# Kernel optimization log

Hardware: AMD Instinct MI355X
Metric: run time of the kernel (lower is better)

Reference implementation:

```python
import jax, jax.numpy as jnp
import numpy as np

B, S, H, NH, EHH, L = 8, 4, 50, 200, 400, 2
HID = 128
FDIM = 44 + 20 + 15          # 79: atom one-hot + amino-acid one-hot + position one-hot
EDIM = 2 * FDIM + 3          # h_i, h_j, distance, bond, t -> 161


def setup_inputs() -> dict:
    key = jax.random.key(0)
    ks = jax.random.split(key, 32)
    inp = {}
    inp["t"] = jax.random.uniform(ks[0], (B,), dtype=jnp.float32)
    inp["x_h"] = jax.random.normal(ks[1], (B, S, H, 3), dtype=jnp.float32)
    inp["x_heavy"] = jax.random.normal(ks[2], (B, 1, NH, 3), dtype=jnp.float32)
    inp["bond_matrix_h_heavy"] = (jax.random.uniform(ks[3], (B, H, NH)) < 0.02).astype(jnp.float32)
    inp["edge_mask_h_heavy"] = jnp.ones((B, H, NH), jnp.float32)
    inp["edge_mask_h_h"] = jnp.ones((B, EHH), jnp.float32)
    inp["atom_mask"] = jnp.ones((B, H, 1), jnp.float32)
    sc = 0.02
    shapes = {"W1": (L, EDIM, HID), "b1": (L, HID), "W2": (L, HID, HID), "b2": (L, HID),
              "Wc1": (L, HID, HID), "bc1": (L, HID), "Wc2": (L, HID, 1),
              "Wn1": (L, FDIM + HID, HID), "bn1": (L, HID), "Wn2": (L, HID, FDIM), "bn2": (L, FDIM)}
    for i, (n, s) in enumerate(shapes.items()):
        inp[n] = jax.random.normal(ks[4 + i], s, dtype=jnp.float32) * sc
    inp["peptide_seq"] = jax.random.randint(ks[20], (B, 15), 0, 20)
    inp["atom_labels_heavy"] = jax.random.randint(ks[21], (B, NH), 0, 44)
    inp["atom_labels_h"] = jax.random.randint(ks[22], (B, H), 0, 44)
    inp["amino_acid_pos_heavy"] = jax.random.randint(ks[23], (B, NH), 1, 16)
    inp["amino_acid_pos_h"] = jax.random.randint(ks[24], (B, H), 1, 16)
    inp["edges_h_h"] = jax.random.randint(ks[25], (B, EHH, 2), 0, H)
    inp["bound_atom"] = jax.random.randint(ks[26], (B, H), 0, NH)
    return inp


def _embed(labels, pos, peptide_seq):
    # one_hot(atom,44) ++ one_hot(seq[pos-1],20) ++ one_hot(pos-1,15)
    aa = jnp.take_along_axis(peptide_seq, pos - 1, axis=1)
    return jnp.concatenate([jax.nn.one_hot(labels, 44, dtype=jnp.float32),
                            jax.nn.one_hot(aa, 20, dtype=jnp.float32),
                            jax.nn.one_hot(pos - 1, 15, dtype=jnp.float32)], axis=-1)


def _gather_nodes(feat, idx):
    # feat [B,S,N,D], idx [B,E] -> [B,S,E,D]
    return jnp.take_along_axis(feat, idx[:, None, :, None], axis=2)


def _seg(data, ids, n):
    # data [B,S,E,D], ids [B,E] -> scatter-add over edges -> [B,S,n,D]
    f = jax.vmap(lambda d, i: jax.ops.segment_sum(jnp.swapaxes(d, 0, 1), i, num_segments=n))
    return jnp.swapaxes(f(data, ids), 1, 2)


def _forward(t, x_h, x_heavy, bond_hm, em_hheavy, em_hh, atom_mask,
             W1, b1, W2, b2, Wc1, bc1, Wc2, Wn1, bn1, Wn2, bn2,
             peptide_seq, atom_labels_heavy, atom_labels_h, pos_heavy, pos_h,
             edges_h_h, bound_atom):
    Bq, Sq, Hq, _ = x_h.shape
    Nh = x_heavy.shape[2]
    xhv = jnp.broadcast_to(x_heavy, (Bq, Sq, Nh, 3))
    emb_h = _embed(atom_labels_h, pos_h, peptide_seq)          # [B,H,79]
    emb_hv = _embed(atom_labels_heavy, pos_heavy, peptide_seq)  # [B,NH,79]
    # absolute coords: x_h relative to its bound heavy atom
    x_h_abs = x_h + jnp.take_along_axis(xhv, bound_atom[:, None, :, None], axis=2)
    x = jnp.concatenate([x_h_abs, xhv], axis=2)                 # [B,S,N,3]
    feat = jnp.concatenate([emb_h, emb_hv], axis=1)             # [B,N,79]
    feat = jnp.broadcast_to(feat[:, None], (Bq, Sq) + feat.shape[1:])
    bond = jnp.concatenate([jnp.zeros((Bq, Hq, Hq), bond_hm.dtype), bond_hm], axis=-1)  # [B,H,N]
    # edge indices: sparse h-h edges, then full h x heavy grid (row-major, cols offset by H)
    grid_r = jnp.repeat(jnp.arange(Hq), Nh)
    grid_c = Hq + jnp.tile(jnp.arange(Nh), Hq)
    edge_row = jnp.concatenate([edges_h_h[..., 0], jnp.broadcast_to(grid_r, (Bq, Hq * Nh))], axis=-1)
    edge_col = jnp.concatenate([edges_h_h[..., 1], jnp.broadcast_to(grid_c, (Bq, Hq * Nh))], axis=-1)
    emask = jnp.concatenate([em_hh, em_hheavy.reshape(Bq, -1)], axis=-1)[:, None, :, None]  # [B,1,E,1]
    bond_e = jax.vmap(lambda bm, r, c: bm[r, c])(bond, edge_row, edge_col)[:, None, :, None]
    x0 = x
    for l in range(W1.shape[0]):
        xi = _gather_nodes(x, edge_row)
        xj = _gather_nodes(x, edge_col)
        diff = xi - xj                                          # [B,S,E,3]
        dist = jnp.linalg.norm(diff, axis=-1, keepdims=True)    # [B,S,E,1]
        hi = _gather_nodes(feat, edge_row)
        hj = _gather_nodes(feat, edge_col)
        t_e = jnp.broadcast_to(t[:, None, None, None], dist.shape)
        ef = jnp.concatenate([hi, hj, dist, jnp.broadcast_to(bond_e, dist.shape), t_e], axis=-1)
        m = jax.nn.silu(ef @ W1[l] + b1[l])
        m = jax.nn.silu(m @ W2[l] + b2[l]) * emask              # masked messages [B,S,E,HID]
        cw = jax.nn.silu(m @ Wc1[l] + bc1[l]) @ Wc2[l]          # [B,S,E,1]
        agg_x = _seg(diff * cw, edge_row, Hq)                   # [B,S,H,3]
        agg_m = _seg(m, edge_row, Hq)                           # [B,S,H,HID]
        h_h = feat[:, :, :Hq]
        h_out = h_h + jax.nn.silu(jnp.concatenate([h_h, agg_m], axis=-1) @ Wn1[l] + bn1[l]) @ Wn2[l] + bn2[l]
        x = jnp.concatenate([x[:, :, :Hq] + agg_x, x[:, :, Hq:]], axis=2)
        feat = jnp.concatenate([h_out, feat[:, :, Hq:]], axis=2)
    pred = (x[:, :, :Hq] - x0[:, :, :Hq]) * atom_mask[:, None, :, :]
    return pred


def reference(t, x_h, x_heavy, bond_matrix_h_heavy, edge_mask_h_heavy, edge_mask_h_h, atom_mask,
              W1, b1, W2, b2, Wc1, bc1, Wc2, Wn1, bn1, Wn2, bn2,
              peptide_seq, atom_labels_heavy, atom_labels_h, amino_acid_pos_heavy, amino_acid_pos_h,
              edges_h_h, bound_atom):
    return _forward(t, x_h, x_heavy, bond_matrix_h_heavy, edge_mask_h_heavy, edge_mask_h_h, atom_mask,
                    W1, b1, W2, b2, Wc1, bc1, Wc2, Wn1, bn1, Wn2, bn2,
                    peptide_seq, atom_labels_heavy, atom_labels_h, amino_acid_pos_heavy, amino_acid_pos_h,
                    edges_h_h, bound_atom)
```

## Files before the change

### kernel.cpp

```cpp
#include <hip/hip_runtime.h>
#include <math.h>

#define B_     8
#define S_     4
#define H_     50
#define NH_    200
#define EHH_   400
#define L_     2
#define HID_   128
#define FDIM_  79
#define EDIM_  161
#define NN_    250
#define NROW_  1600
#define BS_    32
#define FS_    80
#define MSTR_  136
#define NDIM_  207
#define HVB_   1600

#define OFF_FEATH  0
#define OFF_X      128000
#define OFF_X0H    160000
#define OFF_HHCOL  166400
#define OFF_HHEM   169600
#define OFF_HHOFF  172800
#define OFF_AGG0   173312
#define AGGSTRIDE_ 211200
#define OFF_AGG1   384512
#define OFF_HIW1   595712
#define OFF_HJW1   800512
#define OFF_WP     1414912

typedef __attribute__((ext_vector_type(8))) short short8;
typedef __attribute__((ext_vector_type(4))) float f32x4;

__device__ __forceinline__ float silu_(float v) {
    return v * __builtin_amdgcn_rcpf(1.0f + __expf(-v));
}
__device__ __forceinline__ unsigned short f2bf(float f) {
    unsigned int u = __float_as_uint(f);
    unsigned int r = (u + 0x7fffu + ((u >> 16) & 1u)) >> 16;
    return (unsigned short)r;
}

#define HV_BLKS_    1600
#define PACK_BLKS_  256
#define SORT_BLKS_  8
#define HROW_BLKS_  200
#define FEAT_BLKS_  125
#define XI_BLKS_    32
#define SETUP_BLKS_ (HV_BLKS_ + PACK_BLKS_ + SORT_BLKS_ + HROW_BLKS_ + FEAT_BLKS_ + XI_BLKS_)

__global__ __launch_bounds__(256) void k_setup(
    const float* __restrict__ x_h, const float* __restrict__ x_hv,
    const int* __restrict__ bound,
    const int* __restrict__ ehh, const float* __restrict__ em_hh,
    const float* __restrict__ W1, const float* __restrict__ b1,
    const float* __restrict__ t_in,
    const float* __restrict__ W2, const float* __restrict__ Wc1,
    const int* __restrict__ lab_h, const int* __restrict__ pos_h,
    const int* __restrict__ lab_hv, const int* __restrict__ pos_hv,
    const int* __restrict__ pep,
    float* __restrict__ feat_h,
    float* __restrict__ x, float* __restrict__ x0h,
    int* __restrict__ hhcol, float* __restrict__ hhem, int* __restrict__ hhoff,
    float* __restrict__ hiW1, float* __restrict__ hjW1,
    unsigned short* __restrict__ Wp)
{
    int blk = blockIdx.x, t = threadIdx.x;
    if (blk < HV_BLKS_) {
        int g = blk*256 + t;
        int l = g / 204800;
        int r = g - l*204800;
        int node = r >> 7, col = r & 127;
        int b = node / NH_;
        int label = lab_hv[node], pos = pos_hv[node];
        int aa = pep[b*15 + pos - 1];
        const float* W1l = W1 + l*EDIM_*HID_;
        float hj = W1l[(FDIM_ + label)*HID_ + col]
                 + W1l[(FDIM_ + 44 + aa)*HID_ + col]
                 + W1l[(FDIM_ + 64 + pos - 1)*HID_ + col];
        hjW1[(size_t)(HVB_ + l*1600 + node)*HID_ + col] = hj;
        return;
    }
    blk -= HV_BLKS_;
    if (blk < PACK_BLKS_) {
        int g = blk*256 + t;
        int idx = g & 16383;
        int lm  = g >> 14;
        int l = lm >> 1, mat = lm & 1;
        int j   = idx & 7;
        int l15 = (idx >> 3) & 15;
        int qq  = (idx >> 7) & 3;
        int nt  = (idx >> 9) & 7;
        int kc  = (idx >> 12) & 3;
        int n = nt*16 + l15;
        int k = kc*32 + qq*8 + j;
        const float* W = (mat == 0 ? W2 : Wc1) + l*HID_*HID_;
        Wp[g] = f2bf(W[k*HID_ + n]);
        return;
    }
    blk -= PACK_BLKS_;
    if (blk < SORT_BLKS_) {
        int b = blk;
        __shared__ int scnt[64];
        __shared__ int srow[EHH_], scol[EHH_];
        __shared__ float sem[EHH_];
        if (t < 64) scnt[t] = 0;
        __syncthreads();
        for (int e = t; e < EHH_; e += 256) {
            int r = ehh[(b*EHH_ + e)*2 + 0];
            srow[e] = r;
            scol[e] = ehh[(b*EHH_ + e)*2 + 1];
            sem[e]  = em_hh[b*EHH_ + e];
            atomicAdd(&scnt[r], 1);
        }
        __syncthreads();
        if (t == 0) {
            int acc = 0;
            for (int i = 0; i < H_; ++i) { int v = scnt[i]; scnt[i] = acc; acc += v; }
        }
        __syncthreads();
        if (t < 51) hhoff[b*64 + t] = (t < H_) ? scnt[t] : EHH_;
        __syncthreads();
        for (int e = t; e < EHH_; e += 256) {
            int r = srow[e];
            int pos = atomicAdd(&scnt[r], 1);
            hhcol[b*EHH_ + pos] = scol[e];
            hhem [b*EHH_ + pos] = sem[e];
        }
        return;
    }
    blk -= SORT_BLKS_;
    if (blk < HROW_BLKS_) {
        int g = blk*256 + t;
        int node = g >> 7, col = g & 127;
        int b = node / H_;
        int label = lab_h[node], pos = pos_h[node];
        int aa = pep[b*15 + pos - 1];
        const float* W1l = W1;
        float hi = W1l[label*HID_ + col]
                 + W1l[(44 + aa)*HID_ + col]
                 + W1l[(64 + pos - 1)*HID_ + col]
                 + b1[col]
                 + t_in[b] * W1l[160*HID_ + col];
        float hj = W1l[(FDIM_ + label)*HID_ + col]
                 + W1l[(FDIM_ + 44 + aa)*HID_ + col]
                 + W1l[(FDIM_ + 64 + pos - 1)*HID_ + col];
        int h = node % H_;
        #pragma unroll
        for (int s = 0; s < S_; ++s) {
            int row = (b*S_ + s)*H_ + h;
            hiW1[(size_t)row*HID_ + col] = hi;
            hjW1[(size_t)row*HID_ + col] = hj;
        }
        return;
    }
    blk -= HROW_BLKS_;
    if (blk < FEAT_BLKS_) {
        int g = blk*256 + t;
        int node = g / FS_, f = g % FS_;
        int b = node / H_, h = node % H_;
        int label = lab_h[node], pos = pos_h[node];
        int aa = pep[b*15 + pos - 1];
        float v = 0.f;
        if (f < 44)      v = (f == label)          ? 1.0f : 0.0f;
        else if (f < 64) v = ((f - 44) == aa)      ? 1.0f : 0.0f;
        else if (f < 79) v = ((f - 64) == pos - 1) ? 1.0f : 0.0f;
        #pragma unroll
        for (int s = 0; s < S_; ++s)
            feat_h[((b*S_ + s)*H_ + h)*FS_ + f] = v;
        return;
    }
    blk -= FEAT_BLKS_;
    {
        int g = blk*256 + t;
        if (g >= BS_*NN_) return;
        int bs = g / NN_, n = g % NN_;
        int b = bs / S_;
        if (n < H_) {
            int ba = bound[b*H_ + n];
            for (int d = 0; d < 3; ++d) {
                float v = x_h[(bs*H_ + n)*3 + d] + x_hv[(b*NH_ + ba)*3 + d];
                x[g*4 + d] = v;
                x0h[(bs*H_ + n)*4 + d] = v;
            }
        } else {
            int nh = n - H_;
            for (int d = 0; d < 3; ++d) x[g*4 + d] = x_hv[(b*NH_ + nh)*3 + d];
        }
    }
}

__global__ __launch_bounds__(512) void k_edge_mlp(
    const float* __restrict__ x, const float* __restrict__ hiW1,
    const float* __restrict__ hjW1,
    const int* __restrict__ hhcol, const float* __restrict__ hhem,
    const int* __restrict__ hhoff,
    const float* __restrict__ em_hv, const float* __restrict__ bond_in,
    const float* __restrict__ W1,
    const float* __restrict__ b2, const float* __restrict__ bc1,
    const float* __restrict__ Wc2,
    const unsigned short* __restrict__ Wp, int l,
    float* __restrict__ aggx, float* __restrict__ aggm)
{
    __shared__ unsigned short s_wp[2*16384];
    __shared__ unsigned short s_m[8][16][MSTR_];
    __shared__ float s_hi[2][HID_];
    __shared__ float s_cc[5][HID_];
    __shared__ float s_mr[2][4][HID_];
    __shared__ float s_xr[2][4][4];

    const int t = threadIdx.x, lane = t & 63, w = t >> 6;
    const int l15 = lane & 15, q = lane >> 4;
    const int r  = w >> 2;
    const int wr = w & 3;
    const int node0 = blockIdx.x*2;
    const int node  = node0 + r;
    const int bs = node / H_, h = node - bs*H_;
    const int b  = bs / S_;

    {
        const float4* src = (const float4*)(Wp + (size_t)l*32768);
        float4* dst = (float4*)s_wp;
        #pragma unroll
        for (int i = 0; i < 8; ++i) dst[t + i*512] = src[t + i*512];
    }
    const float* W1l = W1 + l*EDIM_*HID_;
    if (t < 128) {
        s_hi[0][t] = hiW1[(size_t)node0*HID_ + t];
    } else if (t < 256) {
        int c = t - 128;
        s_hi[1][c] = hiW1[(size_t)(node0 + 1)*HID_ + c];
    } else if (t < 384) {
        int c = t - 256;
        s_cc[0][c] = W1l[158*HID_ + c];
        s_cc[3][c] = bc1[l*HID_ + c];
    } else {
        int c = t - 384;
        s_cc[1][c] = W1l[159*HID_ + c];
        s_cc[2][c] = b2 [l*HID_ + c];
        s_cc[4][c] = Wc2[l*HID_ + c];
    }

    const int hh0 = hhoff[b*64 + h];
    const int cnt = hhoff[b*64 + h + 1] - hh0;
    const int E   = cnt + NH_;
    const int NT  = (E + 15) >> 4;

    const float xi0 = x[(bs*NN_ + h)*4 + 0];
    const float xi1 = x[(bs*NN_ + h)*4 + 1];
    const float xi2 = x[(bs*NN_ + h)*4 + 2];

    auto gather = [&](int e, float& d0, float& d1, float& d2,
                      float& dist, float& bnd, float& em, int& jj) {
        if (e < E) {
            int col;
            if (e < cnt) {
                col = hhcol[b*EHH_ + hh0 + e];
                em  = hhem [b*EHH_ + hh0 + e];
                jj  = bs*H_ + col;
            } else {
                int cc = e - cnt;
                col = H_ + cc;
                em  = em_hv [(b*H_ + h)*NH_ + cc];
                bnd = bond_in[(b*H_ + h)*NH_ + cc];
                jj  = HVB_ + l*1600 + b*NH_ + cc;
            }
            d0 = xi0 - x[(bs*NN_ + col)*4 + 0];
            d1 = xi1 - x[(bs*NN_ + col)*4 + 1];
            d2 = xi2 - x[(bs*NN_ + col)*4 + 2];
            dist = sqrtf(d0*d0 + d1*d1 + d2*d2);
        }
    };

    float macc[8] = {0.f,0.f,0.f,0.f,0.f,0.f,0.f,0.f};
    float xacc = 0.f;
    __syncthreads();

    float cd0=0.f, cd1=0.f, cd2=0.f, cdist=0.f, cbnd=0.f, cem=0.f;
    int   cjj = bs*H_;
    if (lane < 16) gather(wr*16 + lane, cd0, cd1, cd2, cdist, cbnd, cem, cjj);
    float distb = __shfl(cdist, l15, 64);
    float bndb  = __shfl(cbnd,  l15, 64);
    int   jjb   = __shfl(cjj,   l15, 64);
    float4 pr[8];
    {
        const float* pj = hjW1 + (size_t)jjb*HID_ + q*8;
        #pragma unroll
        for (int kc = 0; kc < 4; ++kc) {
            pr[2*kc]   = *(const float4*)(pj + kc*32);
            pr[2*kc+1] = *(const float4*)(pj + kc*32 + 4);
        }
    }

    for (int ti = wr; ti < NT; ti += 4) {
        const int nx = ti + 4;
        const bool hasNext = (nx < NT);

        float nd0=0.f, nd1=0.f, nd2=0.f, ndist=0.f, nbnd=0.f, nem=0.f;
        int   njj = bs*H_;
        if (hasNext && lane < 16)
            gather(nx*16 + lane, nd0, nd1, nd2, ndist, nbnd, nem, njj);

        short8 afrag[4];
        #pragma unroll
        for (int kc = 0; kc < 4; ++kc) {
            int k0 = kc*32 + q*8;
            float4 c0 = pr[2*kc];
            float4 c1 = pr[2*kc+1];
            float4 h0 = *(const float4*)&s_hi[r][k0];
            float4 h1 = *(const float4*)&s_hi[r][k0 + 4];
            float4 wa0= *(const float4*)&s_cc[0][k0];
            float4 wa1= *(const float4*)&s_cc[0][k0 + 4];
            float4 wb0= *(const float4*)&s_cc[1][k0];
            float4 wb1= *(const float4*)&s_cc[1][k0 + 4];
            short8 fr;
            fr[0] = (short)f2bf(silu_(h0.x + c0.x + distb*wa0.x + bndb*wb0.x));
            fr[1] = (short)f2bf(silu_(h0.y + c0.y + distb*wa0.y + bndb*wb0.y));
            fr[2] = (short)f2bf(silu_(h0.z + c0.z + distb*wa0.z + bndb*wb0.z));
            fr[3] = (short)f2bf(silu_(h0.w + c0.w + distb*wa0.w + bndb*wb0.w));
            fr[4] = (short)f2bf(silu_(h1.x + c1.x + distb*wa1.x + bndb*wb1.x));
            fr[5] = (short)f2bf(silu_(h1.y + c1.y + distb*wa1.y + bndb*wb1.y));
            fr[6] = (short)f2bf(silu_(h1.z + c1.z + distb*wa1.z + bndb*wb1.z));
            fr[7] = (short)f2bf(silu_(h1.w + c1.w + distb*wa1.w + bndb*wb1.w));
            afrag[kc] = fr;
        }

        float ndistb = 0.f, nbndb = 0.f;
        if (hasNext) {
            ndistb = __shfl(ndist, l15, 64);
            nbndb  = __shfl(nbnd,  l15, 64);
            int njjb = __shfl(njj, l15, 64);
            const float* pj = hjW1 + (size_t)njjb*HID_ + q*8;
            #pragma unroll
            for (int kc = 0; kc < 4; ++kc) {
                pr[2*kc]   = *(const float4*)(pj + kc*32);
                pr[2*kc+1] = *(const float4*)(pj + kc*32 + 4);
            }
        }

        float em4[4];
        #pragma unroll
        for (int rr = 0; rr < 4; ++rr) em4[rr] = __shfl(cem, q*4 + rr, 64);
        #pragma unroll
        for (int nt = 0; nt < 8; ++nt) {
            float bias = s_cc[2][nt*16 + l15];
            f32x4 c = {bias, bias, bias, bias};
            #pragma unroll
            for (int kc = 0; kc < 4; ++kc) {
                short8 bf = *(const short8*)&s_wp[((kc*8 + nt)*64 + lane)*8];
                c = __builtin_amdgcn_mfma_f32_16x16x32_bf16(afrag[kc], bf, c, 0, 0, 0);
            }
            #pragma unroll
            for (int rr = 0; rr < 4; ++rr) {
                float mv = silu_(c[rr]) * em4[rr];
                s_m[w][q*4 + rr][nt*16 + l15] = f2bf(mv);
                macc[nt] += mv;
            }
        }
        __builtin_amdgcn_wave_barrier();

        short8 af2[4];
        #pragma unroll
        for (int kc = 0; kc < 4; ++kc)
            af2[kc] = *(const short8*)&s_m[w][l15][kc*32 + q*8];
        float p[4] = {0.f, 0.f, 0.f, 0.f};
        #pragma unroll
        for (int nt = 0; nt < 8; ++nt) {
            float bias = s_cc[3][nt*16 + l15];
            f32x4 c = {bias, bias, bias, bias};
            #pragma unroll
            for (int kc = 0; kc < 4; ++kc) {
                short8 bf = *(const short8*)&s_wp[16384 + ((kc*8 + nt)*64 + lane)*8];
                c = __builtin_amdgcn_mfma_f32_16x16x32_bf16(af2[kc], bf, c, 0, 0, 0);
            }
            float wcv = s_cc[4][nt*16 + l15];
            #pragma unroll
            for (int rr = 0; rr < 4; ++rr)
                p[rr] += silu_(c[rr]) * wcv;
        }
        #pragma unroll
        for (int m = 1; m < 16; m <<= 1) {
            #pragma unroll
            for (int rr = 0; rr < 4; ++rr) p[rr] += __shfl_xor(p[rr], m, 64);
        }
        #pragma unroll
        for (int rr = 0; rr < 4; ++rr) {
            float sd0 = __shfl(cd0, q*4 + rr, 64);
            float sd1 = __shfl(cd1, q*4 + rr, 64);
            float sd2 = __shfl(cd2, q*4 + rr, 64);
            if (l15 < 3) {
                float dsel = (l15 == 0) ? sd0 : ((l15 == 1) ? sd1 : sd2);
                xacc += dsel * p[rr];
            }
        }
        __builtin_amdgcn_wave_barrier();

        cd0 = nd0; cd1 = nd1; cd2 = nd2; cem = nem;
        distb = ndistb; bndb = nbndb;
    }

    #pragma unroll
    for (int nt = 0; nt < 8; ++nt) {
        macc[nt] += __shfl_xor(macc[nt], 16, 64);
        macc[nt] += __shfl_xor(macc[nt], 32, 64);
    }
    if (q == 0) {
        #pragma unroll
        for (int nt = 0; nt < 8; ++nt) s_mr[r][wr][nt*16 + l15] = macc[nt];
    }
    xacc += __shfl_xor(xacc, 16, 64);
    xacc += __shfl_xor(xacc, 32, 64);
    if (q == 0 && l15 < 3) s_xr[r][wr][l15] = xacc;
    __syncthreads();
    if (t < 256) {
        int rr = t >> 7, col = t & 127;
        aggm[(size_t)(node0 + rr)*HID_ + col] =
            s_mr[rr][0][col] + s_mr[rr][1][col] + s_mr[rr][2][col] + s_mr[rr][3][col];
    } else if (t < 262) {
        int ix = t - 256, rr = ix / 3, d = ix - rr*3;
        aggx[(node0 + rr)*4 + d] =
            s_xr[rr][0][d] + s_xr[rr][1][d] + s_xr[rr][2][d] + s_xr[rr][3][d];
    }
}

__global__ __launch_bounds__(128) void k_update(
    float* __restrict__ feat_h, float* __restrict__ x,
    const float* __restrict__ aggm, const float* __restrict__ aggx,
    const float* __restrict__ Wn1, const float* __restrict__ bn1,
    const float* __restrict__ Wn2, const float* __restrict__ bn2, int l,
    const float* __restrict__ W1, const float* __restrict__ b1,
    const float* __restrict__ t_in,
    float* __restrict__ hiW1, float* __restrict__ hjW1, int do_w1,
    const float* __restrict__ x0h, const float* __restrict__ amask,
    float* __restrict__ out)
{
    __shared__ float s_in[8][NDIM_ + 1];
    __shared__ float s_u[8][HID_ + 1];
    int node0 = blockIdx.x * 8;
    int t = threadIdx.x;
    for (int idx = t; idx < 8*(NDIM_ + 1); idx += 128) {
        int g = idx / (NDIM_ + 1), k = idx % (NDIM_ + 1);
        float v = 0.f;
        if (k < FDIM_)      v = feat_h[(node0 + g)*FS_ + k];
        else if (k < NDIM_) v = aggm[(size_t)(node0 + g)*HID_ + (k - FDIM_)];
        s_in[g][k] = v;
    }
    __syncthreads();
    const float* Wn1l = Wn1 + l*NDIM_*HID_;
    float acc[8];
    float bv = bn1[l*HID_ + t];
    #pragma unroll
    for (int g = 0; g < 8; ++g) acc[g] = bv;
    for (int k = 0; k < NDIM_; ++k) {
        float wv = Wn1l[k*HID_ + t];
        #pragma unroll
        for (int g = 0; g < 8; ++g) acc[g] += s_in[g][k] * wv;
    }
    #pragma unroll
    for (int g = 0; g < 8; ++g) s_u[g][t] = silu_(acc[g]);
    __syncthreads();
    if (t < FDIM_) {
        const float* Wn2l = Wn2 + l*HID_*FDIM_;
        float acc2[8];
        float b2v = bn2[l*FDIM_ + t];
        #pragma unroll
        for (int g = 0; g < 8; ++g) acc2[g] = b2v;
        for (int k = 0; k < HID_; ++k) {
            float wv = Wn2l[k*FDIM_ + t];
            #pragma unroll
            for (int g = 0; g < 8; ++g) acc2[g] += s_u[g][k] * wv;
        }
        #pragma unroll
        for (int g = 0; g < 8; ++g) {
            float nf = s_in[g][t] + acc2[g];
            feat_h[(node0 + g)*FS_ + t] = nf;
            s_in[g][t] = nf;
        }
    } else if (t >= 96 && t < 120) {
        int idx = t - 96, g = idx / 3, d = idx % 3;
        int node = node0 + g;
        int bs = node / H_, h = node % H_;
        float xv = x[(bs*NN_ + h)*4 + d] + aggx[node*4 + d];
        x[(bs*NN_ + h)*4 + d] = xv;
        if (!do_w1) {
            int b = bs / S_;
            out[node*3 + d] = (xv - x0h[node*4 + d]) * amask[b*H_ + h];
        }
    }
    if (!do_w1) return;
    __syncthreads();
    {
        const float* W1n = W1 + (l + 1)*EDIM_*HID_;
        float w160 = W1n[160*HID_ + t];
        float b1v  = b1[(l + 1)*HID_ + t];
        float hia[8], hja[8];
        #pragma unroll
        for (int g = 0; g < 8; ++g) { hia[g] = 0.f; hja[g] = 0.f; }
        for (int f = 0; f < FDIM_; ++f) {
            float wi = W1n[f*HID_ + t];
            float wj = W1n[(FDIM_ + f)*HID_ + t];
            #pragma unroll
            for (int g = 0; g < 8; ++g) {
                float v = s_in[g][f];
                hia[g] += v * wi;
                hja[g] += v * wj;
            }
        }
        #pragma unroll
        for (int g = 0; g < 8; ++g) {
            int node = node0 + g;
            int b = (node / H_) / S_;
            hiW1[(size_t)node*HID_ + t] = hia[g] + b1v + t_in[b]*w160;
            hjW1[(size_t)node*HID_ + t] = hja[g];
        }
    }
}

extern "C" void kernel_launch(void* const* d_in, const int* in_sizes, int n_in,
                              void* d_out, int out_size, void* d_ws, size_t ws_size,
                              hipStream_t stream)
{
    const float* t_in  = (const float*)d_in[0];
    const float* x_h   = (const float*)d_in[1];
    const float* x_hv  = (const float*)d_in[2];
    const float* bond  = (const float*)d_in[3];
    const float* em_hv = (const float*)d_in[4];
    const float* em_hh = (const float*)d_in[5];
    const float* amask = (const float*)d_in[6];
    const float* W1    = (const float*)d_in[7];
    const float* b1    = (const float*)d_in[8];
    const float* W2    = (const float*)d_in[9];
    const float* b2    = (const float*)d_in[10];
    const float* Wc1   = (const float*)d_in[11];
    const float* bc1   = (const float*)d_in[12];
    const float* Wc2   = (const float*)d_in[13];
    const float* Wn1   = (const float*)d_in[14];
    const float* bn1   = (const float*)d_in[15];
    const float* Wn2   = (const float*)d_in[16];
    const float* bn2   = (const float*)d_in[17];
    const int* pep     = (const int*)d_in[18];
    const int* lab_hv  = (const int*)d_in[19];
    const int* lab_h   = (const int*)d_in[20];
    const int* pos_hv  = (const int*)d_in[21];
    const int* pos_h   = (const int*)d_in[22];
    const int* ehh     = (const int*)d_in[23];
    const int* bound   = (const int*)d_in[24];

    float* ws     = (float*)d_ws;
    float* feat_h = ws + OFF_FEATH;
    float* x      = ws + OFF_X;
    float* x0h    = ws + OFF_X0H;
    int*   hhcol  = (int*)(ws + OFF_HHCOL);
    float* hhem   = ws + OFF_HHEM;
    int*   hhoff  = (int*)(ws + OFF_HHOFF);
    float* hiW1   = ws + OFF_HIW1;
    float* hjW1   = ws + OFF_HJW1;
    unsigned short* Wp = (unsigned short*)(ws + OFF_WP);

    hipLaunchKernelGGL(k_setup, dim3(SETUP_BLKS_), dim3(256), 0, stream,
                       x_h, x_hv, bound, ehh, em_hh,
                       W1, b1, t_in, W2, Wc1,
                       lab_h, pos_h, lab_hv, pos_hv, pep,
                       feat_h, x, x0h, hhcol, hhem, hhoff,
                       hiW1, hjW1, Wp);

    for (int l = 0; l < L_; ++l) {
        float* aggx_l = ws + OFF_AGG0 + (size_t)l*AGGSTRIDE_;
        float* aggm_l = aggx_l + 6400;
        hipLaunchKernelGGL(k_edge_mlp, dim3(NROW_/2), dim3(512), 0, stream,
                           x, hiW1, hjW1, hhcol, hhem, hhoff, em_hv, bond,
                           W1, b2, bc1, Wc2, Wp, l, aggx_l, aggm_l);
        int do_w1 = (l == 0);
        hipLaunchKernelGGL(k_update, dim3(200), dim3(128), 0, stream,
                           feat_h, x, aggm_l, aggx_l, Wn1, bn1, Wn2, bn2, l,
                           W1, b1, t_in, hiW1, hjW1, do_w1,
                           x0h, amask, (float*)d_out);
    }
}
```

Baseline: 384.9 us.

## Split k_update into more blocks with a two-way K-split reduction

The node-update kernel now handles 4 nodes per block instead of 8, using 256 threads and 400 blocks instead of 200 blocks of 128. The two halves of each block split the reduction dimension of every matmul (Wn1, Wn2 and the next-layer W1 projection) and combine partial sums through shared memory. The aim is more parallelism and occupancy on a small, latency-bound kernel. The cost is extra syncthreads and shared-memory reductions, and each weight row is now read by twice as many blocks.

```diff
diff --git a/kernel.cpp b/kernel.cpp
--- a/kernel.cpp
+++ b/kernel.cpp
@@ -425,7 +425,7 @@
     }
 }
 
-__global__ __launch_bounds__(128) void k_update(
+__global__ __launch_bounds__(256) void k_update(
     float* __restrict__ feat_h, float* __restrict__ x,
     const float* __restrict__ aggm, const float* __restrict__ aggx,
     const float* __restrict__ Wn1, const float* __restrict__ bn1,
@@ -436,11 +436,16 @@
     const float* __restrict__ x0h, const float* __restrict__ amask,
     float* __restrict__ out)
 {
-    __shared__ float s_in[8][NDIM_ + 1];
-    __shared__ float s_u[8][HID_ + 1];
-    int node0 = blockIdx.x * 8;
-    int t = threadIdx.x;
-    for (int idx = t; idx < 8*(NDIM_ + 1); idx += 128) {
+    __shared__ float s_in[4][NDIM_ + 1];
+    __shared__ float s_u [4][HID_ + 1];
+    __shared__ float s_p1[2][4][HID_];
+    __shared__ float s_p2[2][4][HID_];
+    const int node0 = blockIdx.x * 4;
+    const int t = threadIdx.x;
+    const int c  = t & 127;
+    const int kh = t >> 7;
+
+    for (int idx = t; idx < 4*(NDIM_ + 1); idx += 256) {
         int g = idx / (NDIM_ + 1), k = idx % (NDIM_ + 1);
         float v = 0.f;
         if (k < FDIM_)      v = feat_h[(node0 + g)*FS_ + k];
@@ -448,40 +453,53 @@
         s_in[g][k] = v;
     }
     __syncthreads();
-    const float* Wn1l = Wn1 + l*NDIM_*HID_;
-    float acc[8];
-    float bv = bn1[l*HID_ + t];
-    #pragma unroll
-    for (int g = 0; g < 8; ++g) acc[g] = bv;
-    for (int k = 0; k < NDIM_; ++k) {
-        float wv = Wn1l[k*HID_ + t];
-        #pragma unroll
-        for (int g = 0; g < 8; ++g) acc[g] += s_in[g][k] * wv;
-    }
-    #pragma unroll
-    for (int g = 0; g < 8; ++g) s_u[g][t] = silu_(acc[g]);
+
+    {
+        const float* Wn1l = Wn1 + l*NDIM_*HID_;
+        float acc[4] = {0.f, 0.f, 0.f, 0.f};
+        const int k0 = kh*104, k1 = kh ? NDIM_ : 104;
+        for (int k = k0; k < k1; ++k) {
+            float wv = Wn1l[k*HID_ + c];
+            #pragma unroll
+            for (int g = 0; g < 4; ++g) acc[g] += s_in[g][k] * wv;
+        }
+        #pragma unroll
+        for (int g = 0; g < 4; ++g) s_p1[kh][g][c] = acc[g];
+    }
     __syncthreads();
-    if (t < FDIM_) {
+    if (kh == 0) {
+        float bv = bn1[l*HID_ + c];
+        #pragma unroll
+        for (int g = 0; g < 4; ++g)
+            s_u[g][c] = silu_(s_p1[0][g][c] + s_p1[1][g][c] + bv);
+    }
+    __syncthreads();
+
+    if (c < FDIM_) {
         const float* Wn2l = Wn2 + l*HID_*FDIM_;
-        float acc2[8];
-        float b2v = bn2[l*FDIM_ + t];
-        #pragma unroll
-        for (int g = 0; g < 8; ++g) acc2[g] = b2v;
-        for (int k = 0; k < HID_; ++k) {
-            float wv = Wn2l[k*FDIM_ + t];
-            #pragma unroll
-            for (int g = 0; g < 8; ++g) acc2[g] += s_u[g][k] * wv;
-        }
-        #pragma unroll
-        for (int g = 0; g < 8; ++g) {
-            float nf = s_in[g][t] + acc2[g];
-            feat_h[(node0 + g)*FS_ + t] = nf;
-            s_in[g][t] = nf;
-        }
-    } else if (t >= 96 && t < 120) {
-        int idx = t - 96, g = idx / 3, d = idx % 3;
+        float a2[4] = {0.f, 0.f, 0.f, 0.f};
+        const int kk0 = kh*64, kk1 = kk0 + 64;
+        for (int k = kk0; k < kk1; ++k) {
+            float wv = Wn2l[k*FDIM_ + c];
+            #pragma unroll
+            for (int g = 0; g < 4; ++g) a2[g] += s_u[g][k] * wv;
+        }
+        #pragma unroll
+        for (int g = 0; g < 4; ++g) s_p1[kh][g][c] = a2[g];
+    }
+    __syncthreads();
+    if (kh == 0 && c < FDIM_) {
+        float b2v = bn2[l*FDIM_ + c];
+        #pragma unroll
+        for (int g = 0; g < 4; ++g) {
+            float nf = s_in[g][c] + s_p1[0][g][c] + s_p1[1][g][c] + b2v;
+            feat_h[(node0 + g)*FS_ + c] = nf;
+            s_in[g][c] = nf;
+        }
+    } else if (kh == 1 && c < 12) {
+        int g = c / 3, d = c - g*3;
         int node = node0 + g;
-        int bs = node / H_, h = node % H_;
+        int bs = node / H_, h = node - bs*H_;
         float xv = x[(bs*NN_ + h)*4 + d] + aggx[node*4 + d];
         x[(bs*NN_ + h)*4 + d] = xv;
         if (!do_w1) {
@@ -491,29 +509,38 @@
     }
     if (!do_w1) return;
     __syncthreads();
+
     {
         const float* W1n = W1 + (l + 1)*EDIM_*HID_;
-        float w160 = W1n[160*HID_ + t];
-        float b1v  = b1[(l + 1)*HID_ + t];
-        float hia[8], hja[8];
-        #pragma unroll
-        for (int g = 0; g < 8; ++g) { hia[g] = 0.f; hja[g] = 0.f; }
-        for (int f = 0; f < FDIM_; ++f) {
-            float wi = W1n[f*HID_ + t];
-            float wj = W1n[(FDIM_ + f)*HID_ + t];
-            #pragma unroll
-            for (int g = 0; g < 8; ++g) {
+        float hia[4] = {0.f,0.f,0.f,0.f}, hja[4] = {0.f,0.f,0.f,0.f};
+        const int f0 = kh*40, f1 = kh ? FDIM_ : 40;
+        for (int f = f0; f < f1; ++f) {
+            float wi = W1n[f*HID_ + c];
+            float wj = W1n[(FDIM_ + f)*HID_ + c];
+            #pragma unroll
+            for (int g = 0; g < 4; ++g) {
                 float v = s_in[g][f];
                 hia[g] += v * wi;
                 hja[g] += v * wj;
             }
         }
         #pragma unroll
-        for (int g = 0; g < 8; ++g) {
-            int node = node0 + g;
-            int b = (node / H_) / S_;
-            hiW1[(size_t)node*HID_ + t] = hia[g] + b1v + t_in[b]*w160;
-            hjW1[(size_t)node*HID_ + t] = hja[g];
+        for (int g = 0; g < 4; ++g) {
+            s_p1[kh][g][c] = hia[g];
+            s_p2[kh][g][c] = hja[g];
+        }
+        __syncthreads();
+        if (kh == 0) {
+            float w160 = W1n[160*HID_ + c];
+            float b1v  = b1[(l + 1)*HID_ + c];
+            #pragma unroll
+            for (int g = 0; g < 4; ++g) {
+                int node = node0 + g;
+                int b = (node / H_) / S_;
+                hiW1[(size_t)node*HID_ + c] =
+                    s_p1[0][g][c] + s_p1[1][g][c] + b1v + t_in[b]*w160;
+                hjW1[(size_t)node*HID_ + c] = s_p2[0][g][c] + s_p2[1][g][c];
+            }
         }
     }
 }
@@ -573,7 +600,7 @@
                            x, hiW1, hjW1, hhcol, hhem, hhoff, em_hv, bond,
                            W1, b2, bc1, Wc2, Wp, l, aggx_l, aggm_l);
         int do_w1 = (l == 0);
-        hipLaunchKernelGGL(k_update, dim3(200), dim3(128), 0, stream,
+        hipLaunchKernelGGL(k_update, dim3(400), dim3(256), 0, stream,
                            feat_h, x, aggm_l, aggx_l, Wn1, bn1, Wn2, bn2, l,
                            W1, b1, t_in, hiW1, hjW1, do_w1,
                            x0h, amask, (float*)d_out);
```

Measured after the change: 383.7 us. No clear change (-0.3%).

## Fuse node update into edge MLP kernel with double-buffered coordinates

Applied to the files above, without the earlier changes.

Merges the per-node update (Wn1/Wn2 MLP, coordinate update, next-layer W1 projections) into the tail of the edge kernel, so each layer is one launch. Aggregated messages feed the node MLP directly from shared memory instead of a global round-trip. Coordinates and the hi/hj projection buffers are double-buffered per layer to avoid read-after-write races across blocks. The cost is small per-block node work on 512 threads with extra syncs, and the update is spread over 800 blocks of 2 nodes instead of 200 blocks of 8, so weight reads are repeated more often.

```diff
diff --git a/kernel.cpp b/kernel.cpp
--- a/kernel.cpp
+++ b/kernel.cpp
@@ -19,17 +19,15 @@
 #define HVB_   1600
 
 #define OFF_FEATH  0
-#define OFF_X      128000
-#define OFF_X0H    160000
-#define OFF_HHCOL  166400
-#define OFF_HHEM   169600
-#define OFF_HHOFF  172800
-#define OFF_AGG0   173312
-#define AGGSTRIDE_ 211200
-#define OFF_AGG1   384512
-#define OFF_HIW1   595712
-#define OFF_HJW1   800512
-#define OFF_WP     1414912
+#define OFF_X0     128000
+#define OFF_X1     160000
+#define OFF_X0H    192000
+#define OFF_HHCOL  198400
+#define OFF_HHEM   201600
+#define OFF_HHOFF  204800
+#define OFF_HIW1   205312
+#define OFF_HJW1   614912
+#define OFF_WP     1434112
 
 typedef __attribute__((ext_vector_type(8))) short short8;
 typedef __attribute__((ext_vector_type(4))) float f32x4;
@@ -62,7 +60,7 @@
     const int* __restrict__ lab_hv, const int* __restrict__ pos_hv,
     const int* __restrict__ pep,
     float* __restrict__ feat_h,
-    float* __restrict__ x, float* __restrict__ x0h,
+    float* __restrict__ x0, float* __restrict__ x1, float* __restrict__ x0h,
     int* __restrict__ hhcol, float* __restrict__ hhem, int* __restrict__ hhoff,
     float* __restrict__ hiW1, float* __restrict__ hjW1,
     unsigned short* __restrict__ Wp)
@@ -182,18 +180,22 @@
             int ba = bound[b*H_ + n];
             for (int d = 0; d < 3; ++d) {
                 float v = x_h[(bs*H_ + n)*3 + d] + x_hv[(b*NH_ + ba)*3 + d];
-                x[g*4 + d] = v;
+                x0[g*4 + d] = v;
                 x0h[(bs*H_ + n)*4 + d] = v;
             }
         } else {
             int nh = n - H_;
-            for (int d = 0; d < 3; ++d) x[g*4 + d] = x_hv[(b*NH_ + nh)*3 + d];
+            for (int d = 0; d < 3; ++d) {
+                float v = x_hv[(b*NH_ + nh)*3 + d];
+                x0[g*4 + d] = v;
+                x1[g*4 + d] = v;
+            }
         }
     }
 }
 
 __global__ __launch_bounds__(512) void k_edge_mlp(
-    const float* __restrict__ x, const float* __restrict__ hiW1,
+    const float* __restrict__ xin, const float* __restrict__ hiW1g,
     const float* __restrict__ hjW1,
     const int* __restrict__ hhcol, const float* __restrict__ hhem,
     const int* __restrict__ hhoff,
@@ -202,7 +204,13 @@
     const float* __restrict__ b2, const float* __restrict__ bc1,
     const float* __restrict__ Wc2,
     const unsigned short* __restrict__ Wp, int l,
-    float* __restrict__ aggx, float* __restrict__ aggm)
+    const float* __restrict__ Wn1, const float* __restrict__ bn1,
+    const float* __restrict__ Wn2, const float* __restrict__ bn2,
+    const float* __restrict__ b1, const float* __restrict__ t_in,
+    float* __restrict__ feat_h, float* __restrict__ xout,
+    float* __restrict__ hiW1w, float* __restrict__ hjW1w,
+    const float* __restrict__ x0h, const float* __restrict__ amask,
+    float* __restrict__ out, int do_w1)
 {
     __shared__ unsigned short s_wp[2*16384];
     __shared__ unsigned short s_m[8][16][MSTR_];
@@ -219,6 +227,7 @@
     const int node  = node0 + r;
     const int bs = node / H_, h = node - bs*H_;
     const int b  = bs / S_;
+    const int hb = (l ? 4800 : 0) + bs*H_;
 
     {
         const float4* src = (const float4*)(Wp + (size_t)l*32768);
@@ -228,10 +237,10 @@
     }
     const float* W1l = W1 + l*EDIM_*HID_;
     if (t < 128) {
-        s_hi[0][t] = hiW1[(size_t)node0*HID_ + t];
+        s_hi[0][t] = hiW1g[(size_t)(l*1600 + node0)*HID_ + t];
     } else if (t < 256) {
         int c = t - 128;
-        s_hi[1][c] = hiW1[(size_t)(node0 + 1)*HID_ + c];
+        s_hi[1][c] = hiW1g[(size_t)(l*1600 + node0 + 1)*HID_ + c];
     } else if (t < 384) {
         int c = t - 256;
         s_cc[0][c] = W1l[158*HID_ + c];
@@ -248,9 +257,9 @@
     const int E   = cnt + NH_;
     const int NT  = (E + 15) >> 4;
 
-    const float xi0 = x[(bs*NN_ + h)*4 + 0];
-    const float xi1 = x[(bs*NN_ + h)*4 + 1];
-    const float xi2 = x[(bs*NN_ + h)*4 + 2];
+    const float xi0 = xin[(bs*NN_ + h)*4 + 0];
+    const float xi1 = xin[(bs*NN_ + h)*4 + 1];
+    const float xi2 = xin[(bs*NN_ + h)*4 + 2];
 
     auto gather = [&](int e, float& d0, float& d1, float& d2,
                       float& dist, float& bnd, float& em, int& jj) {
@@ -259,7 +268,7 @@
             if (e < cnt) {
                 col = hhcol[b*EHH_ + hh0 + e];
                 em  = hhem [b*EHH_ + hh0 + e];
-                jj  = bs*H_ + col;
+                jj  = hb + col;
             } else {
                 int cc = e - cnt;
                 col = H_ + cc;
@@ -267,9 +276,9 @@
                 bnd = bond_in[(b*H_ + h)*NH_ + cc];
                 jj  = HVB_ + l*1600 + b*NH_ + cc;
             }
-            d0 = xi0 - x[(bs*NN_ + col)*4 + 0];
-            d1 = xi1 - x[(bs*NN_ + col)*4 + 1];
-            d2 = xi2 - x[(bs*NN_ + col)*4 + 2];
+            d0 = xi0 - xin[(bs*NN_ + col)*4 + 0];
+            d1 = xi1 - xin[(bs*NN_ + col)*4 + 1];
+            d2 = xi2 - xin[(bs*NN_ + col)*4 + 2];
             dist = sqrtf(d0*d0 + d1*d1 + d2*d2);
         }
     };
@@ -279,7 +288,7 @@
     __syncthreads();
 
     float cd0=0.f, cd1=0.f, cd2=0.f, cdist=0.f, cbnd=0.f, cem=0.f;
-    int   cjj = bs*H_;
+    int   cjj = hb;
     if (lane < 16) gather(wr*16 + lane, cd0, cd1, cd2, cdist, cbnd, cem, cjj);
     float distb = __shfl(cdist, l15, 64);
     float bndb  = __shfl(cbnd,  l15, 64);
@@ -299,7 +308,7 @@
         const bool hasNext = (nx < NT);
 
         float nd0=0.f, nd1=0.f, nd2=0.f, ndist=0.f, nbnd=0.f, nem=0.f;
-        int   njj = bs*H_;
+        int   njj = hb;
         if (hasNext && lane < 16)
             gather(nx*16 + lane, nd0, nd1, nd2, ndist, nbnd, nem, njj);
 
@@ -414,106 +423,79 @@
     xacc += __shfl_xor(xacc, 32, 64);
     if (q == 0 && l15 < 3) s_xr[r][wr][l15] = xacc;
     __syncthreads();
-    if (t < 256) {
-        int rr = t >> 7, col = t & 127;
-        aggm[(size_t)(node0 + rr)*HID_ + col] =
-            s_mr[rr][0][col] + s_mr[rr][1][col] + s_mr[rr][2][col] + s_mr[rr][3][col];
-    } else if (t < 262) {
-        int ix = t - 256, rr = ix / 3, d = ix - rr*3;
-        aggx[(node0 + rr)*4 + d] =
-            s_xr[rr][0][d] + s_xr[rr][1][d] + s_xr[rr][2][d] + s_xr[rr][3][d];
-    }
-}
-
-__global__ __launch_bounds__(128) void k_update(
-    float* __restrict__ feat_h, float* __restrict__ x,
-    const float* __restrict__ aggm, const float* __restrict__ aggx,
-    const float* __restrict__ Wn1, const float* __restrict__ bn1,
-    const float* __restrict__ Wn2, const float* __restrict__ bn2, int l,
-    const float* __restrict__ W1, const float* __restrict__ b1,
-    const float* __restrict__ t_in,
-    float* __restrict__ hiW1, float* __restrict__ hjW1, int do_w1,
-    const float* __restrict__ x0h, const float* __restrict__ amask,
-    float* __restrict__ out)
-{
-    __shared__ float s_in[8][NDIM_ + 1];
-    __shared__ float s_u[8][HID_ + 1];
-    int node0 = blockIdx.x * 8;
-    int t = threadIdx.x;
-    for (int idx = t; idx < 8*(NDIM_ + 1); idx += 128) {
-        int g = idx / (NDIM_ + 1), k = idx % (NDIM_ + 1);
+
+    float* su = (float*)s_wp;
+    if (t < 416) {
+        int g = t / 208, k = t - g*208;
         float v = 0.f;
         if (k < FDIM_)      v = feat_h[(node0 + g)*FS_ + k];
-        else if (k < NDIM_) v = aggm[(size_t)(node0 + g)*HID_ + (k - FDIM_)];
-        s_in[g][k] = v;
-    }
-    __syncthreads();
-    const float* Wn1l = Wn1 + l*NDIM_*HID_;
-    float acc[8];
-    float bv = bn1[l*HID_ + t];
-    #pragma unroll
-    for (int g = 0; g < 8; ++g) acc[g] = bv;
-    for (int k = 0; k < NDIM_; ++k) {
-        float wv = Wn1l[k*HID_ + t];
-        #pragma unroll
-        for (int g = 0; g < 8; ++g) acc[g] += s_in[g][k] * wv;
-    }
-    #pragma unroll
-    for (int g = 0; g < 8; ++g) s_u[g][t] = silu_(acc[g]);
-    __syncthreads();
-    if (t < FDIM_) {
+        else if (k < NDIM_) {
+            int c = k - FDIM_;
+            v = s_mr[g][0][c] + s_mr[g][1][c] + s_mr[g][2][c] + s_mr[g][3][c];
+        }
+        su[g*208 + k] = v;
+    }
+    __syncthreads();
+    {
+        const float* Wn1l = Wn1 + l*NDIM_*HID_;
+        int kh = t >> 8, g = (t >> 7) & 1, c = t & 127;
+        int k0 = kh*104, k1 = kh ? NDIM_ : 104;
+        float acc = 0.f;
+        for (int k = k0; k < k1; ++k)
+            acc += su[g*208 + k] * Wn1l[k*HID_ + c];
+        su[1024 + t] = acc;
+    }
+    __syncthreads();
+    if (t < 256) {
+        int c = t & 127;
+        su[512 + t] = silu_(su[1024 + t] + su[1280 + t] + bn1[l*HID_ + c]);
+    }
+    __syncthreads();
+    if (t < 316) {
         const float* Wn2l = Wn2 + l*HID_*FDIM_;
-        float acc2[8];
-        float b2v = bn2[l*FDIM_ + t];
-        #pragma unroll
-        for (int g = 0; g < 8; ++g) acc2[g] = b2v;
-        for (int k = 0; k < HID_; ++k) {
-            float wv = Wn2l[k*FDIM_ + t];
-            #pragma unroll
-            for (int g = 0; g < 8; ++g) acc2[g] += s_u[g][k] * wv;
-        }
-        #pragma unroll
-        for (int g = 0; g < 8; ++g) {
-            float nf = s_in[g][t] + acc2[g];
-            feat_h[(node0 + g)*FS_ + t] = nf;
-            s_in[g][t] = nf;
-        }
-    } else if (t >= 96 && t < 120) {
-        int idx = t - 96, g = idx / 3, d = idx % 3;
-        int node = node0 + g;
-        int bs = node / H_, h = node % H_;
-        float xv = x[(bs*NN_ + h)*4 + d] + aggx[node*4 + d];
-        x[(bs*NN_ + h)*4 + d] = xv;
-        if (!do_w1) {
-            int b = bs / S_;
-            out[node*3 + d] = (xv - x0h[node*4 + d]) * amask[b*H_ + h];
+        int kh = t / 158, r2 = t - kh*158;
+        int g = r2 / FDIM_, c = r2 - g*FDIM_;
+        int kk0 = kh*64, kk1 = kk0 + 64;
+        float acc = 0.f;
+        for (int k = kk0; k < kk1; ++k)
+            acc += su[512 + g*HID_ + k] * Wn2l[k*FDIM_ + c];
+        su[1536 + t] = acc;
+    }
+    __syncthreads();
+    if (t < 158) {
+        int g = t / FDIM_, c = t - g*FDIM_;
+        float nf = su[g*208 + c] + su[1536 + t] + su[1694 + t] + bn2[l*FDIM_ + c];
+        feat_h[(node0 + g)*FS_ + c] = nf;
+        su[g*208 + c] = nf;
+    } else if (t >= 256 && t < 262) {
+        int ix = t - 256, g = ix / 3, d = ix - g*3;
+        int ng = node0 + g;
+        int bsg = ng / H_, hg = ng - bsg*H_;
+        float xv = xin[(bsg*NN_ + hg)*4 + d]
+                 + s_xr[g][0][d] + s_xr[g][1][d] + s_xr[g][2][d] + s_xr[g][3][d];
+        if (do_w1) {
+            xout[(bsg*NN_ + hg)*4 + d] = xv;
+        } else {
+            int bg = bsg / S_;
+            out[ng*3 + d] = (xv - x0h[ng*4 + d]) * amask[bg*H_ + hg];
         }
     }
     if (!do_w1) return;
     __syncthreads();
     {
-        const float* W1n = W1 + (l + 1)*EDIM_*HID_;
-        float w160 = W1n[160*HID_ + t];
-        float b1v  = b1[(l + 1)*HID_ + t];
-        float hia[8], hja[8];
-        #pragma unroll
-        for (int g = 0; g < 8; ++g) { hia[g] = 0.f; hja[g] = 0.f; }
-        for (int f = 0; f < FDIM_; ++f) {
-            float wi = W1n[f*HID_ + t];
-            float wj = W1n[(FDIM_ + f)*HID_ + t];
-            #pragma unroll
-            for (int g = 0; g < 8; ++g) {
-                float v = s_in[g][f];
-                hia[g] += v * wi;
-                hja[g] += v * wj;
-            }
-        }
-        #pragma unroll
-        for (int g = 0; g < 8; ++g) {
-            int node = node0 + g;
-            int b = (node / H_) / S_;
-            hiW1[(size_t)node*HID_ + t] = hia[g] + b1v + t_in[b]*w160;
-            hjW1[(size_t)node*HID_ + t] = hja[g];
+        const float* W1n = W1 + EDIM_*HID_;
+        int sel = t >> 8, g = (t >> 7) & 1, c = t & 127;
+        int base = sel ? FDIM_ : 0;
+        float acc = 0.f;
+        for (int f = 0; f < FDIM_; ++f)
+            acc += su[g*208 + f] * W1n[(base + f)*HID_ + c];
+        int ng = node0 + g;
+        if (sel == 0) {
+            int bg = (ng / H_) / S_;
+            hiW1w[(size_t)(1600 + ng)*HID_ + c] =
+                acc + b1[HID_ + c] + t_in[bg]*W1n[160*HID_ + c];
+        } else {
+            hjW1w[(size_t)(4800 + ng)*HID_ + c] = acc;
         }
     }
 }
@@ -550,7 +532,8 @@
 
     float* ws     = (float*)d_ws;
     float* feat_h = ws + OFF_FEATH;
-    float* x      = ws + OFF_X;
+    float* x0     = ws + OFF_X0;
+    float* x1     = ws + OFF_X1;
     float* x0h    = ws + OFF_X0H;
     int*   hhcol  = (int*)(ws + OFF_HHCOL);
     float* hhem   = ws + OFF_HHEM;
@@ -563,19 +546,20 @@
                        x_h, x_hv, bound, ehh, em_hh,
                        W1, b1, t_in, W2, Wc1,
                        lab_h, pos_h, lab_hv, pos_hv, pep,
-                       feat_h, x, x0h, hhcol, hhem, hhoff,
+                       feat_h, x0, x1, x0h, hhcol, hhem, hhoff,
                        hiW1, hjW1, Wp);
 
-    for (int l = 0; l < L_; ++l) {
-        float* aggx_l = ws + OFF_AGG0 + (size_t)l*AGGSTRIDE_;
-        float* aggm_l = aggx_l + 6400;
-        hipLaunchKernelGGL(k_edge_mlp, dim3(NROW_/2), dim3(512), 0, stream,
-                           x, hiW1, hjW1, hhcol, hhem, hhoff, em_hv, bond,
-                           W1, b2, bc1, Wc2, Wp, l, aggx_l, aggm_l);
-        int do_w1 = (l == 0);
-        hipLaunchKernelGGL(k_update, dim3(200), dim3(128), 0, stream,
-                           feat_h, x, aggm_l, aggx_l, Wn1, bn1, Wn2, bn2, l,
-                           W1, b1, t_in, hiW1, hjW1, do_w1,
-                           x0h, amask, (float*)d_out);
-    }
+    hipLaunchKernelGGL(k_edge_mlp, dim3(NROW_/2), dim3(512), 0, stream,
+                       x0, hiW1, hjW1, hhcol, hhem, hhoff, em_hv, bond,
+                       W1, b2, bc1, Wc2, Wp, 0,
+                       Wn1, bn1, Wn2, bn2, b1, t_in,
+                       feat_h, x1, hiW1, hjW1, x0h, amask,
+                       (float*)d_out, 1);
+
+    hipLaunchKernelGGL(k_edge_mlp, dim3(NROW_/2), dim3(512), 0, stream,
+                       x1, hiW1, hjW1, hhcol, hhem, hhoff, em_hv, bond,
+                       W1, b2, bc1, Wc2, Wp, 1,
+                       Wn1, bn1, Wn2, bn2, b1, t_in,
+                       feat_h, x1, hiW1, hjW1, x0h, amask,
+                       (float*)d_out, 0);
 }
```

Result: slower. 443.4 us (+15.2%).
